# Kernel tuning notes

Hardware: AMD Instinct MI355X
Metric: run time of the kernel (lower is better)

Reference implementation:

```python
import jax, jax.numpy as jnp
import numpy as np

B, N, K, F, S = 128, 116, 4, 72, 8
TOPK = 10
INTRA_T, INTER_T = 0.1, 0.2


def _safe_corr(f):
    # f: [batch, d, m] -> corr [batch, d, d], matching torch _safe_compute_correlation
    c = f - f.mean(axis=2, keepdims=True)
    cov = jnp.einsum('bim,bjm->bij', c, c)
    var = jnp.diagonal(cov, axis1=1, axis2=2)
    std = jnp.sqrt(jnp.clip(var, 1e-8, None))[:, :, None]
    corr = cov / (std * std.transpose(0, 2, 1) + 1e-8)
    return jnp.clip(corr, -1.0, 1.0)


def _sym(m):
    return (m + m.swapaxes(-1, -2)) * 0.5


def setup_inputs():
    key = jax.random.key(0)
    ks = jax.random.split(key, 8)
    def lin(k, out_d, in_d):
        return jax.random.normal(k, (out_d, in_d), jnp.float32) * (1.0 / np.sqrt(in_d))
    return {
        'band_features': jax.random.normal(ks[0], (B, N, K, F), jnp.float32),
        'attn_weights': jax.random.uniform(ks[1], (B, N, S, K), jnp.float32),
        'intra_thresh_adj': jnp.zeros((), jnp.float32),
        'inter_thresh_adj': jnp.zeros((), jnp.float32),
        'attn_fuse_weight': jnp.asarray(0.5, jnp.float32),
        'intra_W1': lin(ks[2], 64, N), 'intra_b1': jnp.zeros((64,), jnp.float32),
        'intra_W2': lin(ks[3], N, 64), 'intra_b2': jnp.zeros((N,), jnp.float32),
        'inter_W1': lin(ks[4], 32, K), 'inter_b1': jnp.zeros((32,), jnp.float32),
        'inter_W2': lin(ks[5], K, 32), 'inter_b2': jnp.zeros((K,), jnp.float32),
        'comp_W': lin(ks[6], 128, 2 * F + 6), 'comp_b': jnp.zeros((128,), jnp.float32),
    }


def reference(band_features, attn_weights, intra_thresh_adj, inter_thresh_adj,
              attn_fuse_weight, intra_W1, intra_b1, intra_W2, intra_b2,
              inter_W1, inter_b1, inter_W2, inter_b2, comp_W, comp_b):
    dt = band_features.dtype
    # ---- intra-band graph: [B*K, N, N] correlations ----
    x = band_features.transpose(0, 2, 1, 3).reshape(B * K, N, F)
    corr = _safe_corr(x)
    th = INTRA_T + jax.nn.sigmoid(intra_thresh_adj) * 0.2
    tmask = (jnp.abs(corr) > th).astype(dt)
    _, idx = jax.lax.top_k(jnp.abs(corr), min(TOPK, N))  # [B*K, N, k]
    bix = jnp.arange(B * K)[:, None, None]
    rix = jnp.arange(N)[None, :, None]
    kmask = jnp.zeros_like(corr).at[bix, rix, idx].set(1.0)
    sc = jax.nn.relu(_sym(corr * tmask * kmask))
    h = jax.nn.relu(sc.reshape(-1, N) @ intra_W1.T + intra_b1)  # dropout = eval identity
    intra = jax.nn.sigmoid(h @ intra_W2.T + intra_b2).reshape(B * K, N, N)
    intra_adj = _sym(intra).reshape(B, K, N, N)
    # ---- inter-band graph: [B*N, K, K] correlations ----
    y = band_features.reshape(B * N, K, F)
    base = _safe_corr(y)
    a = attn_weights.reshape(B * N, S, K).transpose(0, 2, 1)  # [B*N, K, S]
    acorr = _safe_corr(a)
    fw = jax.nn.sigmoid(attn_fuse_weight)
    base = fw * base + (1.0 - fw) * acorr
    th2 = INTER_T + jax.nn.sigmoid(inter_thresh_adj) * 0.2
    sc2 = jax.nn.relu(_sym(base * (jnp.abs(base) > th2).astype(dt)))
    h2 = jax.nn.relu(sc2.reshape(-1, K) @ inter_W1.T + inter_b1)
    inter = jax.nn.sigmoid(h2 @ inter_W2.T + inter_b2).reshape(B * N, K, K)
    inter_adj = _sym(inter).reshape(B, N, K, K)
    # ---- unified graph assembly (vectorized replacement of nested loops) ----
    kk = jnp.arange(K)
    bd = jnp.zeros((B, K, N, K, N), dt).at[:, kk, :, kk, :].set(
        intra_adj.transpose(1, 0, 2, 3))  # block-diagonal intra blocks
    unified = bd.reshape(B, K * N, K * N)
    kk1, kk2, nn = np.meshgrid(np.arange(K), np.arange(K), np.arange(N), indexing='ij')
    sel = (kk1 != kk2).ravel()
    k1f, k2f, nf = kk1.ravel()[sel], kk2.ravel()[sel], nn.ravel()[sel]
    vals = inter_adj[:, nf, k1f, k2f]  # [B, M]
    unified_adj = unified.at[:, k1f * N + nf, k2f * N + nf].set(vals)
    # ---- node features ----
    node_features = band_features.transpose(0, 2, 1, 3).reshape(B, K * N, F)
    # ---- graph-level features ----
    node_mean = band_features.mean(axis=(1, 2))
    node_std = jnp.std(band_features, axis=(1, 2), ddof=1)  # torch unbiased std
    deg = (intra_adj > 0).astype(dt).sum(axis=3)  # [B, K, N]
    tri = jnp.einsum('bkij,bkji->bki', intra_adj, intra_adj)  # diag of A@A
    clus = tri / (deg ** 2 + 1e-8)
    dens = (inter_adj > 0).astype(dt).mean(axis=(2, 3))  # [B, N]
    stren = inter_adj.mean(axis=(2, 3))
    gf = jnp.concatenate([
        node_mean, node_std,
        deg.mean(axis=(1, 2))[:, None], jnp.std(deg, axis=(1, 2), ddof=1)[:, None],
        clus.mean(axis=(1, 2))[:, None], jnp.std(clus, axis=(1, 2), ddof=1)[:, None],
        dens.mean(axis=1)[:, None], stren.mean(axis=1)[:, None]], axis=1)
    graph_features = jax.nn.relu(gf @ comp_W.T + comp_b)
    # ---- sparsity scalars ----
    intra_sp = 1.0 - (intra_adj > 0).astype(dt).mean()
    inter_sp = 1.0 - (inter_adj > 0).astype(dt).mean()
    it, jt = float(B * K * N * N), float(B * N * K * K)
    total_sp = (intra_sp * it + inter_sp * jt) / (it + jt)
    return (unified_adj, node_features, graph_features, intra_adj, inter_adj,
            intra_sp, inter_sp, total_sp)
```

## Files before the change

kernel.cpp:

```cpp
#include <hip/hip_runtime.h>
#include <math.h>

#define NB 128
#define NN_ 116
#define NK 4
#define NF 72
#define NS 8
#define TOPK 10

#define BK (NB*NK)
#define BN (NB*NN_)
#define NN2 (NN_*NN_)
#define KN (NK*NN_)
#define ROWS (BK*NN_)

#define OFF_UNI 0
#define SZ_UNI (NB*KN*KN)
#define OFF_NF (OFF_UNI + SZ_UNI)
#define SZ_NF (NB*KN*NF)
#define OFF_GF (OFF_NF + SZ_NF)
#define SZ_GF (NB*128)
#define OFF_IA (OFF_GF + SZ_GF)
#define SZ_IA (NB*NK*NN_*NN_)
#define OFF_IE (OFF_IA + SZ_IA)
#define SZ_IE (NB*NN_*NK*NK)
#define OFF_SP (OFF_IE + SZ_IE)

#define SCR_CORR 0
#define SCR_DEG (SCR_CORR + SZ_IA)
#define SCR_CLUS (SCR_DEG + ROWS)
#define SCR_DENS (SCR_CLUS + ROWS)
#define SCR_STREN (SCR_DENS + BN)
#define SCR_AUX (SCR_STREN + BN)

#define NFQ (SZ_NF/4)
#define UNQ (SZ_UNI/4)
#define NB_CORR 512
#define NB_INTER (BN/64)
#define NB_COPY 1044

__device__ __forceinline__ float sigmoidf_(float x){ return 1.0f/(1.0f+expf(-x)); }
__device__ __forceinline__ float dot4_(float4 a, float4 b){
    return fmaf(a.x,b.x, fmaf(a.y,b.y, fmaf(a.z,b.z, a.w*b.w)));
}
#define CLIP1(x) fminf(1.0f, fmaxf(-1.0f, (x)))

__global__ __launch_bounds__(256, 1) void k_corr_inter(const float* __restrict__ band,
    const float* __restrict__ attn, const float* __restrict__ thadj2,
    const float* __restrict__ fwp,
    const float* __restrict__ eW1, const float* __restrict__ eb1,
    const float* __restrict__ eW2, const float* __restrict__ eb2,
    float* __restrict__ corr_out, float* __restrict__ inter_out,
    float* __restrict__ dens_out, float* __restrict__ stren_out,
    float* __restrict__ nf)
{
    __shared__ float sx[NF*120];
    __shared__ float smu[120], srs[120];
    __shared__ float sW1[128], sb1[32], sW2[128], sb2[4];
    __shared__ float sMat[256*4];
    int t = threadIdx.x;
    if (blockIdx.x < NB_CORR){
        int bk = blockIdx.x;
        int b = bk >> 2, k = bk & 3;
        const float* xin = band + ((size_t)b*NN_*NK + k)*NF;
        for (int e = t; e < NN_*NF; e += 256){
            int n = e / NF, f = e - n*NF;
            sx[f*120 + n] = xin[(size_t)n*NK*NF + f];
        }
        for (int e = t; e < NF*4; e += 256)
            sx[(e>>2)*120 + NN_ + (e&3)] = 0.0f;
        __syncthreads();
        if (t < NN_){
            float s = 0.f, ss = 0.f;
            for (int f = 0; f < NF; ++f){ float v = sx[f*120+t]; s += v; ss += v*v; }
            float mu = s * (1.0f/NF);
            float sd = sqrtf(fmaxf(ss - s*mu, 1e-8f));
            smu[t] = mu; srs[t] = 1.0f/sd;
        }
        __syncthreads();
        for (int e = t; e < NF*NN_; e += 256){
            int f = e / NN_, n = e - f*NN_;
            sx[f*120+n] = (sx[f*120+n] - smu[n]) * srs[n];
        }
        __syncthreads();
        float* dst = corr_out + (size_t)bk * NN2;
        if (t < 225){
            int ti = t / 15, tj = t - ti*15;
            int i0 = ti*8, j0 = tj*8;
            float acc[8][8] = {};
            for (int f = 0; f < NF; ++f){
                const float4 a0 = *(const float4*)&sx[f*120 + i0];
                const float4 a1 = *(const float4*)&sx[f*120 + i0 + 4];
                const float4 c0 = *(const float4*)&sx[f*120 + j0];
                const float4 c1 = *(const float4*)&sx[f*120 + j0 + 4];
                float av[8] = {a0.x,a0.y,a0.z,a0.w,a1.x,a1.y,a1.z,a1.w};
                float cv[8] = {c0.x,c0.y,c0.z,c0.w,c1.x,c1.y,c1.z,c1.w};
                #pragma unroll
                for (int r = 0; r < 8; ++r)
                    #pragma unroll
                    for (int c = 0; c < 8; ++c)
                        acc[r][c] = fmaf(av[r], cv[c], acc[r][c]);
            }
            #pragma unroll
            for (int r = 0; r < 8; ++r){
                int i = i0 + r;
                if (i < NN_){
                    float4 v0;
                    v0.x = CLIP1(acc[r][0]); v0.y = CLIP1(acc[r][1]);
                    v0.z = CLIP1(acc[r][2]); v0.w = CLIP1(acc[r][3]);
                    *(float4*)&dst[i*NN_ + j0] = v0;
                    if (j0 + 4 <= 112){
                        float4 v1;
                        v1.x = CLIP1(acc[r][4]); v1.y = CLIP1(acc[r][5]);
                        v1.z = CLIP1(acc[r][6]); v1.w = CLIP1(acc[r][7]);
                        *(float4*)&dst[i*NN_ + j0 + 4] = v1;
                    }
                }
            }
        }
    } else if (blockIdx.x < NB_CORR + NB_INTER){
        if (t < 128) sW1[t] = eW1[t];
        if (t < 32) sb1[t] = eb1[t];
        if (t >= 128 && t < 256) sW2[t-128] = eW2[t-128];
        if (t < 4) sb2[t] = eb2[t];
        __syncthreads();
        int l = t & 3;
        int il = t >> 2;
        size_t item = (size_t)(blockIdx.x - NB_CORR)*64 + il;

        const float* xr = band + item*(NK*NF) + l*NF;
        float s=0,p0=0,p1=0,p2=0,p3=0;
        for (int f = 0; f < NF; ++f){
            float v = xr[f];
            float v1=__shfl_xor(v,1), v2=__shfl_xor(v,2), v3=__shfl_xor(v,3);
            s += v; p0=fmaf(v,v,p0); p1=fmaf(v,v1,p1); p2=fmaf(v,v2,p2); p3=fmaf(v,v3,p3);
        }
        float mu = s*(1.0f/NF);
        float mu1=__shfl_xor(mu,1), mu2=__shfl_xor(mu,2), mu3=__shfl_xor(mu,3);
        float sd = sqrtf(fmaxf(p0 - s*mu, 1e-8f));
        float sd1=__shfl_xor(sd,1), sd2=__shfl_xor(sd,2), sd3=__shfl_xor(sd,3);
        float c0 = CLIP1((p0 - (float)NF*mu*mu )/(sd*sd +1e-8f));
        float c1 = CLIP1((p1 - (float)NF*mu*mu1)/(sd*sd1+1e-8f));
        float c2 = CLIP1((p2 - (float)NF*mu*mu2)/(sd*sd2+1e-8f));
        float c3 = CLIP1((p3 - (float)NF*mu*mu3)/(sd*sd3+1e-8f));

        const float* ar = attn + item*(NS*NK) + l;
        float as=0,q0=0,q1=0,q2=0,q3=0;
        #pragma unroll
        for (int s8 = 0; s8 < NS; ++s8){
            float v = ar[s8*NK];
            float v1=__shfl_xor(v,1), v2=__shfl_xor(v,2), v3=__shfl_xor(v,3);
            as += v; q0=fmaf(v,v,q0); q1=fmaf(v,v1,q1); q2=fmaf(v,v2,q2); q3=fmaf(v,v3,q3);
        }
        float am = as*(1.0f/NS);
        float am1=__shfl_xor(am,1), am2=__shfl_xor(am,2), am3=__shfl_xor(am,3);
        float ad = sqrtf(fmaxf(q0 - as*am, 1e-8f));
        float ad1=__shfl_xor(ad,1), ad2=__shfl_xor(ad,2), ad3=__shfl_xor(ad,3);
        float a0 = CLIP1((q0 - (float)NS*am*am )/(ad*ad +1e-8f));
        float a1 = CLIP1((q1 - (float)NS*am*am1)/(ad*ad1+1e-8f));
        float a2 = CLIP1((q2 - (float)NS*am*am2)/(ad*ad2+1e-8f));
        float a3 = CLIP1((q3 - (float)NS*am*am3)/(ad*ad3+1e-8f));

        float fwv = sigmoidf_(fwp[0]);
        float g0 = fwv*c0 + (1.0f-fwv)*a0;
        float g1 = fwv*c1 + (1.0f-fwv)*a1;
        float g2 = fwv*c2 + (1.0f-fwv)*a2;
        float g3 = fwv*c3 + (1.0f-fwv)*a3;
        float th2 = 0.2f + sigmoidf_(thadj2[0])*0.2f;
        float m0 = (fabsf(g0)>th2)?g0:0.f;
        float m1 = (fabsf(g1)>th2)?g1:0.f;
        float m2 = (fabsf(g2)>th2)?g2:0.f;
        float m3 = (fabsf(g3)>th2)?g3:0.f;

        sMat[il*16 + l*4 + (l^0)] = m0;
        sMat[il*16 + l*4 + (l^1)] = m1;
        sMat[il*16 + l*4 + (l^2)] = m2;
        sMat[il*16 + l*4 + (l^3)] = m3;
        __syncthreads();
        float x0 = fmaxf(0.5f*(sMat[il*16 + l*4 + 0] + sMat[il*16 + 0*4 + l]), 0.f);
        float x1 = fmaxf(0.5f*(sMat[il*16 + l*4 + 1] + sMat[il*16 + 1*4 + l]), 0.f);
        float x2 = fmaxf(0.5f*(sMat[il*16 + l*4 + 2] + sMat[il*16 + 2*4 + l]), 0.f);
        float x3 = fmaxf(0.5f*(sMat[il*16 + l*4 + 3] + sMat[il*16 + 3*4 + l]), 0.f);

        float h[32];
        #pragma unroll
        for (int o = 0; o < 32; ++o){
            float acc = sb1[o];
            acc = fmaf(sW1[o*4+0], x0, acc);
            acc = fmaf(sW1[o*4+1], x1, acc);
            acc = fmaf(sW1[o*4+2], x2, acc);
            acc = fmaf(sW1[o*4+3], x3, acc);
            h[o] = fmaxf(acc, 0.f);
        }
        float o0=sb2[0], o1=sb2[1], o2=sb2[2], o3=sb2[3];
        #pragma unroll
        for (int o = 0; o < 32; ++o){
            float hv = h[o];
            o0 = fmaf(sW2[0*32+o], hv, o0);
            o1 = fmaf(sW2[1*32+o], hv, o1);
            o2 = fmaf(sW2[2*32+o], hv, o2);
            o3 = fmaf(sW2[3*32+o], hv, o3);
        }
        o0 = sigmoidf_(o0); o1 = sigmoidf_(o1); o2 = sigmoidf_(o2); o3 = sigmoidf_(o3);
        __syncthreads();
        sMat[il*16 + l*4 + 0] = o0;
        sMat[il*16 + l*4 + 1] = o1;
        sMat[il*16 + l*4 + 2] = o2;
        sMat[il*16 + l*4 + 3] = o3;
        __syncthreads();
        float y0 = 0.5f*(o0 + sMat[il*16 + 0*4 + l]);
        float y1 = 0.5f*(o1 + sMat[il*16 + 1*4 + l]);
        float y2 = 0.5f*(o2 + sMat[il*16 + 2*4 + l]);
        float y3 = 0.5f*(o3 + sMat[il*16 + 3*4 + l]);
        *(float4*)&inter_out[item*16 + l*4] = make_float4(y0,y1,y2,y3);

        float cnt = ((y0>0.f)?1.f:0.f) + ((y1>0.f)?1.f:0.f) + ((y2>0.f)?1.f:0.f) + ((y3>0.f)?1.f:0.f);
        float sum = y0+y1+y2+y3;
        cnt += __shfl_xor(cnt,1); cnt += __shfl_xor(cnt,2);
        sum += __shfl_xor(sum,1); sum += __shfl_xor(sum,2);
        if (l == 0){
            dens_out[item]  = cnt * (1.0f/16.0f);
            stren_out[item] = sum * (1.0f/16.0f);
        }
    } else {
        int gid = (blockIdx.x - NB_CORR - NB_INTER)*256 + t;
        int gsz = NB_COPY*256;
        for (int q = gid; q < NFQ; q += gsz){
            int fq = q % 18;
            int rest = q / 18;
            int b = rest / KN;
            int p = rest - b*KN;
            int k = p / NN_;
            int n = p - k*NN_;
            float4 v = *(const float4*)&band[(((size_t)b*NN_ + n)*NK + k)*NF + fq*4];
            *(float4*)&nf[(size_t)q*4] = v;
        }
    }
}

__global__ __launch_bounds__(1024, 1) void k_topk_mlpsym(const float* __restrict__ corr,
    const float* __restrict__ thadj,
    const float* __restrict__ W1, const float* __restrict__ b1,
    const float* __restrict__ W2, const float* __restrict__ b2,
    float* __restrict__ ia, float* __restrict__ deg_out, float* __restrict__ clus_out)
{
    __shared__ float smem[38708];
    float* sA  = smem;
    float* sB  = smem + 14036;
    float* sW2 = smem + 21460;
    float* sH  = smem + 30164;
    float* sb1 = smem + 38052;
    float* sb2 = smem + 38116;
    unsigned* sKm  = (unsigned*)(smem + 38244);
    unsigned* sTop = (unsigned*)sH;
    int bk = blockIdx.x, t = threadIdx.x;

    const float* src = corr + (size_t)bk*NN2;
    for (int e4 = t; e4 < NN2/4; e4 += 1024){
        int e = e4*4;
        int i = e / 116, j = e - i*116;
        float4 v = *(const float4*)&src[e];
        sA[i*121 + j + 0] = v.x;
        sA[i*121 + j + 1] = v.y;
        sA[i*121 + j + 2] = v.z;
        sA[i*121 + j + 3] = v.w;
    }
    for (int e4 = t; e4 < 1856; e4 += 1024)
        *(float4*)&sB[e4*4] = *(const float4*)&W1[e4*4];
    for (int e = t; e < 128*64; e += 1024){
        int j = e >> 6, o = e & 63;
        sW2[j*68 + o] = (j < NN_) ? W2[e] : 0.0f;
    }
    if (t < 64) sb1[t] = b1[t];
    if (t >= 64 && t < 192) sb2[t-64] = (t-64 < NN_) ? b2[t-64] : 0.0f;
    __syncthreads();

    if (t < 464){
        int r = t >> 2, q = t & 3;
        const float* row = &sA[r*121 + q*29];
        int jbase = q*29;
        unsigned tv[TOPK];
        #pragma unroll
        for (int p = 0; p < TOPK; ++p) tv[p] = 0u;
        for (int jj = 0; jj < 29; ++jj){
            float c = fabsf(row[jj]);
            unsigned u = (__float_as_uint(c) & 0xFFFFFF80u) | (unsigned)(127 - (jbase + jj));
            #pragma unroll
            for (int p = 0; p < TOPK; ++p){
                unsigned old = tv[p];
                bool gt = u > old;
                tv[p] = gt ? u : old;
                u = gt ? old : u;
            }
        }
        #pragma unroll
        for (int p = 0; p < TOPK; ++p) sTop[t*10 + p] = tv[p];
    }
    __syncthreads();

    if (t < NN_){
        const unsigned* L0 = &sTop[(4*t+0)*10];
        const unsigned* L1 = &sTop[(4*t+1)*10];
        const unsigned* L2 = &sTop[(4*t+2)*10];
        const unsigned* L3 = &sTop[(4*t+3)*10];
        int i0=0, i1=0, i2=0, i3=0;
        unsigned m0=0,m1=0,m2=0,m3=0;
        #pragma unroll
        for (int p = 0; p < TOPK; ++p){
            unsigned u0 = L0[i0], u1 = L1[i1], u2 = L2[i2], u3 = L3[i3];
            unsigned ua = u0 > u1 ? u0 : u1;
            unsigned ub = u2 > u3 ? u2 : u3;
            unsigned u  = ua > ub ? ua : ub;
            if (u == u0) ++i0; else if (u == u1) ++i1; else if (u == u2) ++i2; else ++i3;
            int j = 127 - (int)(u & 127u);
            unsigned bit = 1u << (j & 31);
            int w = j >> 5;
            if (w == 0) m0 |= bit; else if (w == 1) m1 |= bit; else if (w == 2) m2 |= bit; else m3 |= bit;
        }
        sKm[t*4+0]=m0; sKm[t*4+1]=m1; sKm[t*4+2]=m2; sKm[t*4+3]=m3;
    }
    __syncthreads();

    {
        float th = 0.1f + sigmoidf_(thadj[0]) * 0.2f;
        float vb[14];
        #pragma unroll
        for (int it = 0; it < 14; ++it){
            int e = t + it*1024;
            float v = 0.0f;
            if (e < NN2){
                int i = e / 116, j = e - i*116;
                float cij = sA[i*121 + j];
                float cji = sA[j*121 + i];
                bool kij = (sKm[i*4 + (j>>5)] >> (j&31)) & 1u;
                bool kji = (sKm[j*4 + (i>>5)] >> (i&31)) & 1u;
                float mij = (fabsf(cij) > th && kij) ? cij : 0.0f;
                float mji = (fabsf(cji) > th && kji) ? cji : 0.0f;
                v = fmaxf(0.5f*(mij+mji), 0.0f);
            }
            vb[it] = v;
        }
        __syncthreads();
        #pragma unroll
        for (int it = 0; it < 14; ++it){
            int e = t + it*1024;
            if (e < NN2) sA[e] = vb[it];
        }
    }
    __syncthreads();

    if (t < 928){
        int rg = t >> 4, og = t & 15;
        float acc[2][4] = {};
        for (int j4 = 0; j4 < 29; ++j4){
            float4 s[2], w[4];
            #pragma unroll
            for (int m = 0; m < 2; ++m) s[m] = *(const float4*)&sA[(rg+58*m)*116 + j4*4];
            #pragma unroll
            for (int n = 0; n < 4; ++n) w[n] = *(const float4*)&sB[(og+16*n)*116 + j4*4];
            #pragma unroll
            for (int m = 0; m < 2; ++m)
                #pragma unroll
                for (int n = 0; n < 4; ++n)
                    acc[m][n] += dot4_(s[m], w[n]);
        }
        #pragma unroll
        for (int m = 0; m < 2; ++m)
            #pragma unroll
            for (int n = 0; n < 4; ++n)
                sH[(rg+58*m)*68 + og+16*n] = fmaxf(acc[m][n] + sb1[og+16*n], 0.0f);
    }
    __syncthreads();

    if (t < 928){
        int rg = t >> 4, jg = t & 15;
        float acc[2][8] = {};
        for (int o4 = 0; o4 < 16; ++o4){
            float4 h[2], w[8];
            #pragma unroll
            for (int m = 0; m < 2; ++m) h[m] = *(const float4*)&sH[(rg+58*m)*68 + o4*4];
            #pragma unroll
            for (int q = 0; q < 8; ++q) w[q] = *(const float4*)&sW2[(jg+16*q)*68 + o4*4];
            #pragma unroll
            for (int m = 0; m < 2; ++m)
                #pragma unroll
                for (int q = 0; q < 8; ++q)
                    acc[m][q] += dot4_(h[m], w[q]);
        }
        #pragma unroll
        for (int m = 0; m < 2; ++m){
            int row = rg + 58*m;
            #pragma unroll
            for (int q = 0; q < 8; ++q){
                int j = jg + 16*q;
                if (j < NN_)
                    sA[row*121 + j] = sigmoidf_(acc[m][q] + sb2[j]);
            }
        }
    }
    __syncthreads();

    float* dia = ia + (size_t)bk*NN2;
    for (int e4 = t; e4 < NN2/4; e4 += 1024){
        int e = e4*4;
        int i = e / 116, j0 = e - i*116;
        float4 v;
        v.x = 0.5f*(sA[i*121+j0+0] + sA[(j0+0)*121+i]);
        v.y = 0.5f*(sA[i*121+j0+1] + sA[(j0+1)*121+i]);
        v.z = 0.5f*(sA[i*121+j0+2] + sA[(j0+2)*121+i]);
        v.w = 0.5f*(sA[i*121+j0+3] + sA[(j0+3)*121+i]);
        *(float4*)&dia[e] = v;
    }
    if (t < 464){
        int r = t >> 2, q = t & 3;
        float tri = 0.f, dg = 0.f;
        for (int jj = 0; jj < 29; ++jj){
            int j = q*29 + jj;
            float v = 0.5f*(sA[r*121+j] + sA[j*121+r]);
            tri = fmaf(v, v, tri);
            dg += (v > 0.f) ? 1.f : 0.f;
        }
        tri += __shfl_xor(tri,1); tri += __shfl_xor(tri,2);
        dg  += __shfl_xor(dg,1);  dg  += __shfl_xor(dg,2);
        if (q == 0){
            deg_out[(size_t)bk*NN_ + r]  = dg;
            clus_out[(size_t)bk*NN_ + r] = tri / (dg*dg + 1e-8f);
        }
    }
}

__global__ __launch_bounds__(256) void k_gstats_lin(const float* __restrict__ band,
    const float* __restrict__ deg, const float* __restrict__ clus,
    const float* __restrict__ dens, const float* __restrict__ stren,
    const float* __restrict__ Wc, const float* __restrict__ bc,
    float* __restrict__ gfo, float* __restrict__ aux)
{
    int b = blockIdx.x, t = threadIdx.x;
    __shared__ float sGf[152];
    __shared__ float sPs[18*14*4];
    __shared__ float sPq[18*14*4];
    __shared__ float sA[4], sB[4];

    if (t < 252){
        int fq = t % 18, g = t / 18;
        float4 s = make_float4(0,0,0,0), q = make_float4(0,0,0,0);
        const float* base = band + (size_t)b*(KN*NF);
        for (int nk = g; nk < KN; nk += 14){
            float4 v = *(const float4*)&base[nk*NF + fq*4];
            s.x += v.x; s.y += v.y; s.z += v.z; s.w += v.w;
            q.x = fmaf(v.x,v.x,q.x); q.y = fmaf(v.y,v.y,q.y);
            q.z = fmaf(v.z,v.z,q.z); q.w = fmaf(v.w,v.w,q.w);
        }
        int idx = (fq*14 + g)*4;
        *(float4*)&sPs[idx] = s;
        *(float4*)&sPq[idx] = q;
    }
    __syncthreads();
    if (t < NF){
        int fq = t >> 2, e = t & 3;
        float S = 0.f, Q = 0.f;
        for (int g = 0; g < 14; ++g){ S += sPs[(fq*14+g)*4+e]; Q += sPq[(fq*14+g)*4+e]; }
        float mean = S * (1.0f/(float)KN);
        float var = fmaxf((Q - S*mean)/((float)KN - 1.0f), 0.0f);
        sGf[t] = mean;
        sGf[NF + t] = sqrtf(var);
    }
    __syncthreads();

    float s = 0.f, ss = 0.f;
    for (int e = t; e < KN; e += 256){ float v = deg[(size_t)b*KN + e]; s += v; ss += v*v; }
    #pragma unroll
    for (int d = 1; d < 64; d <<= 1){ s += __shfl_xor(s,d); ss += __shfl_xor(ss,d); }
    if ((t & 63) == 0){ sA[t>>6] = s; sB[t>>6] = ss; }
    __syncthreads();
    if (t == 0){
        float S0 = sA[0]+sA[1]+sA[2]+sA[3], S1 = sB[0]+sB[1]+sB[2]+sB[3];
        float Mv = (float)KN, mean = S0/Mv;
        float var = fmaxf((S1 - S0*mean)/(Mv - 1.0f), 0.0f);
        sGf[144] = mean; sGf[145] = sqrtf(var);
        aux[b] = S0;
    }
    __syncthreads();

    s = 0.f; ss = 0.f;
    for (int e = t; e < KN; e += 256){ float v = clus[(size_t)b*KN + e]; s += v; ss += v*v; }
    #pragma unroll
    for (int d = 1; d < 64; d <<= 1){ s += __shfl_xor(s,d); ss += __shfl_xor(ss,d); }
    if ((t & 63) == 0){ sA[t>>6] = s; sB[t>>6] = ss; }
    __syncthreads();
    if (t == 0){
        float S0 = sA[0]+sA[1]+sA[2]+sA[3], S1 = sB[0]+sB[1]+sB[2]+sB[3];
        float Mv = (float)KN, mean = S0/Mv;
        float var = fmaxf((S1 - S0*mean)/(Mv - 1.0f), 0.0f);
        sGf[146] = mean; sGf[147] = sqrtf(var);
    }
    __syncthreads();

    s = 0.f; ss = 0.f;
    for (int e = t; e < NN_; e += 256){ s += dens[(size_t)b*NN_ + e]; ss += stren[(size_t)b*NN_ + e]; }
    #pragma unroll
    for (int d = 1; d < 64; d <<= 1){ s += __shfl_xor(s,d); ss += __shfl_xor(ss,d); }
    if ((t & 63) == 0){ sA[t>>6] = s; sB[t>>6] = ss; }
    __syncthreads();
    if (t == 0){
        float S0 = sA[0]+sA[1]+sA[2]+sA[3], S1 = sB[0]+sB[1]+sB[2]+sB[3];
        sGf[148] = S0 / (float)NN_;
        sGf[149] = S1 / (float)NN_;
        aux[128 + b] = S0 * 16.0f;
    }
    __syncthreads();

    if (t < 128){
        float acc = bc[t];
        const float* w = Wc + (size_t)t*150;
        for (int c = 0; c < 150; ++c) acc = fmaf(sGf[c], w[c], acc);
        gfo[(size_t)b*128 + t] = fmaxf(acc, 0.f);
    }
}

__global__ __launch_bounds__(64) void k_sparsity(const float* __restrict__ aux, float* __restrict__ out3)
{
    int t = threadIdx.x;
    float a = aux[t] + aux[64 + t];
    float c = aux[128 + t] + aux[192 + t];
    #pragma unroll
    for (int d = 1; d < 64; d <<= 1){ a += __shfl_xor(a,d); c += __shfl_xor(c,d); }
    if (t == 0){
        const float it = 6889472.0f, jt = 237568.0f;
        float isp = 1.0f - a/it;
        float jsp = 1.0f - c/jt;
        out3[0] = isp; out3[1] = jsp;
        out3[2] = (isp*it + jsp*jt)/(it + jt);
    }
}

__global__ __launch_bounds__(256) void k_uninf(const float* __restrict__ intra_adj,
    const float* __restrict__ inter_adj, const float* __restrict__ aux,
    float* __restrict__ uni, float* __restrict__ sp, int do_sp)
{
    if (do_sp && blockIdx.x == 0 && threadIdx.x < 64){
        int t = threadIdx.x;
        float a = aux[t] + aux[64 + t];
        float c = aux[128 + t] + aux[192 + t];
        #pragma unroll
        for (int d = 1; d < 64; d <<= 1){ a += __shfl_xor(a,d); c += __shfl_xor(c,d); }
        if (t == 0){
            const float it = 6889472.0f, jt = 237568.0f;
            float isp = 1.0f - a/it;
            float jsp = 1.0f - c/jt;
            sp[0] = isp; sp[1] = jsp;
            sp[2] = (isp*it + jsp*jt)/(it + jt);
        }
    }
    int gid = blockIdx.x*256 + threadIdx.x;
    int gsz = gridDim.x*256;
    for (int q = gid; q < UNQ; q += gsz){
        int row = q / 116;
        int cq  = q - row*116;
        int b = row / KN;
        int p = row - b*KN;
        int k1 = p / NN_;
        int i  = p - k1*NN_;
        int k2 = cq / 29;
        int j0 = cq*4 - k2*NN_;
        float4 v;
        if (k2 == k1){
            v = *(const float4*)&intra_adj[(((size_t)b*NK + k1)*NN_ + i)*NN_ + j0];
        } else {
            int d = i - j0;
            float val = 0.f;
            if (d >= 0 && d < 4)
                val = inter_adj[(((size_t)b*NN_ + i)*NK + k1)*NK + k2];
            v.x = (d==0)?val:0.f;
            v.y = (d==1)?val:0.f;
            v.z = (d==2)?val:0.f;
            v.w = (d==3)?val:0.f;
        }
        *(float4*)&uni[(size_t)q*4] = v;
    }
}

extern "C" void kernel_launch(void* const* d_in, const int* in_sizes, int n_in,
                              void* d_out, int out_size, void* d_ws, size_t ws_size,
                              hipStream_t stream)
{
    const float* band = (const float*)d_in[0];
    const float* attn = (const float*)d_in[1];
    const float* thA  = (const float*)d_in[2];
    const float* thE  = (const float*)d_in[3];
    const float* fw   = (const float*)d_in[4];
    const float* iW1  = (const float*)d_in[5];
    const float* ib1  = (const float*)d_in[6];
    const float* iW2  = (const float*)d_in[7];
    const float* ib2  = (const float*)d_in[8];
    const float* eW1  = (const float*)d_in[9];
    const float* eb1  = (const float*)d_in[10];
    const float* eW2  = (const float*)d_in[11];
    const float* eb2  = (const float*)d_in[12];
    const float* cW   = (const float*)d_in[13];
    const float* cb   = (const float*)d_in[14];

    float* out = (float*)d_out;
    float* uni = out + OFF_UNI;
    float* nf  = out + OFF_NF;
    float* gfo = out + OFF_GF;
    float* ia  = out + OFF_IA;
    float* ie  = out + OFF_IE;
    float* sp  = out + OFF_SP;

    float* scr_corr  = uni + SCR_CORR;
    float* scr_deg   = uni + SCR_DEG;
    float* scr_clus  = uni + SCR_CLUS;
    float* scr_dens  = uni + SCR_DENS;
    float* scr_stren = uni + SCR_STREN;

    int ws_ok = (ws_size >= 256*sizeof(float));
    float* aux = ws_ok ? (float*)d_ws : (uni + SCR_AUX);

    k_corr_inter<<<NB_CORR + NB_INTER + NB_COPY, 256, 0, stream>>>(
        band, attn, thE, fw, eW1, eb1, eW2, eb2,
        scr_corr, ie, scr_dens, scr_stren, nf);
    k_topk_mlpsym<<<BK, 1024, 0, stream>>>(scr_corr, thA, iW1, ib1, iW2, ib2,
                                           ia, scr_deg, scr_clus);
    k_gstats_lin<<<NB, 256, 0, stream>>>(band, scr_deg, scr_clus, scr_dens, scr_stren,
                                         cW, cb, gfo, aux);
    if (!ws_ok)
        k_sparsity<<<1, 64, 0, stream>>>(aux, sp);
    k_uninf<<<2048, 256, 0, stream>>>(ia, ie, aux, uni, sp, ws_ok ? 1 : 0);
}
```

Baseline: 140.0 us.

## Split-K the intra MLP matmuls across thread pairs with padded LDS strides

The two small per-graph MLP matmuls in the top-k/MLP kernel now give each thread a 4-row register tile (instead of 2) and split the reduction dimension between adjacent lanes, combined with a shuffle-xor. W1 and W2 shared-memory rows are padded (120 and 76 floats) to change bank mapping. This is meant to increase register-level reuse of weight loads and reduce LDS traffic and bank conflicts. In exchange it needs more registers per thread in a 1024-thread block and adds shuffle reductions.

Measured after the change: 144.6 us. 3.3% more time.

```diff
diff --git a/kernel.cpp b/kernel.cpp
--- a/kernel.cpp
+++ b/kernel.cpp
@@ -244,14 +244,14 @@
     const float* __restrict__ W2, const float* __restrict__ b2,
     float* __restrict__ ia, float* __restrict__ deg_out, float* __restrict__ clus_out)
 {
-    __shared__ float smem[38708];
+    __shared__ float smem[39988];
     float* sA  = smem;
-    float* sB  = smem + 14036;
-    float* sW2 = smem + 21460;
-    float* sH  = smem + 30164;
-    float* sb1 = smem + 38052;
-    float* sb2 = smem + 38116;
-    unsigned* sKm  = (unsigned*)(smem + 38244);
+    float* sW1 = smem + 14036;
+    float* sW2 = smem + 21716;
+    float* sH  = smem + 31444;
+    float* sb1 = smem + 39332;
+    float* sb2 = smem + 39396;
+    unsigned* sKm  = (unsigned*)(smem + 39524);
     unsigned* sTop = (unsigned*)sH;
     int bk = blockIdx.x, t = threadIdx.x;
 
@@ -265,11 +265,14 @@
         sA[i*121 + j + 2] = v.z;
         sA[i*121 + j + 3] = v.w;
     }
-    for (int e4 = t; e4 < 1856; e4 += 1024)
-        *(float4*)&sB[e4*4] = *(const float4*)&W1[e4*4];
+    for (int e4 = t; e4 < 1856; e4 += 1024){
+        int e = e4*4;
+        int o = e / 116, j = e - o*116;
+        *(float4*)&sW1[o*120 + j] = *(const float4*)&W1[e];
+    }
     for (int e = t; e < 128*64; e += 1024){
         int j = e >> 6, o = e & 63;
-        sW2[j*68 + o] = (j < NN_) ? W2[e] : 0.0f;
+        sW2[j*76 + o] = (j < NN_) ? W2[e] : 0.0f;
     }
     if (t < 64) sb1[t] = b1[t];
     if (t >= 64 && t < 192) sb2[t-64] = (t-64 < NN_) ? b2[t-64] : 0.0f;
@@ -350,51 +353,69 @@
     __syncthreads();
 
     if (t < 928){
-        int rg = t >> 4, og = t & 15;
-        float acc[2][4] = {};
-        for (int j4 = 0; j4 < 29; ++j4){
-            float4 s[2], w[4];
-            #pragma unroll
-            for (int m = 0; m < 2; ++m) s[m] = *(const float4*)&sA[(rg+58*m)*116 + j4*4];
-            #pragma unroll
-            for (int n = 0; n < 4; ++n) w[n] = *(const float4*)&sB[(og+16*n)*116 + j4*4];
-            #pragma unroll
-            for (int m = 0; m < 2; ++m)
+        int base = t >> 1, kh = t & 1;
+        int rg = base >> 4, og = base & 15;
+        int j4b = kh ? 15 : 0, j4e = kh ? 29 : 15;
+        float acc[4][4] = {};
+        for (int j4 = j4b; j4 < j4e; ++j4){
+            float4 s[4], w[4];
+            #pragma unroll
+            for (int m = 0; m < 4; ++m) s[m] = *(const float4*)&sA[(rg+29*m)*116 + j4*4];
+            #pragma unroll
+            for (int n = 0; n < 4; ++n) w[n] = *(const float4*)&sW1[(og+16*n)*120 + j4*4];
+            #pragma unroll
+            for (int m = 0; m < 4; ++m)
                 #pragma unroll
                 for (int n = 0; n < 4; ++n)
                     acc[m][n] += dot4_(s[m], w[n]);
         }
         #pragma unroll
-        for (int m = 0; m < 2; ++m)
+        for (int m = 0; m < 4; ++m)
             #pragma unroll
             for (int n = 0; n < 4; ++n)
-                sH[(rg+58*m)*68 + og+16*n] = fmaxf(acc[m][n] + sb1[og+16*n], 0.0f);
+                acc[m][n] += __shfl_xor(acc[m][n], 1);
+        if (kh == 0){
+            #pragma unroll
+            for (int m = 0; m < 4; ++m)
+                #pragma unroll
+                for (int n = 0; n < 4; ++n)
+                    sH[(rg+29*m)*68 + og+16*n] = fmaxf(acc[m][n] + sb1[og+16*n], 0.0f);
+        }
     }
     __syncthreads();
 
     if (t < 928){
-        int rg = t >> 4, jg = t & 15;
-        float acc[2][8] = {};
-        for (int o4 = 0; o4 < 16; ++o4){
-            float4 h[2], w[8];
-            #pragma unroll
-            for (int m = 0; m < 2; ++m) h[m] = *(const float4*)&sH[(rg+58*m)*68 + o4*4];
-            #pragma unroll
-            for (int q = 0; q < 8; ++q) w[q] = *(const float4*)&sW2[(jg+16*q)*68 + o4*4];
-            #pragma unroll
-            for (int m = 0; m < 2; ++m)
+        int base = t >> 1, kh = t & 1;
+        int rg = base >> 4, jg = base & 15;
+        int o4b = kh * 8;
+        float acc[4][8] = {};
+        for (int o4 = o4b; o4 < o4b + 8; ++o4){
+            float4 h[4], w[8];
+            #pragma unroll
+            for (int m = 0; m < 4; ++m) h[m] = *(const float4*)&sH[(rg+29*m)*68 + o4*4];
+            #pragma unroll
+            for (int q = 0; q < 8; ++q) w[q] = *(const float4*)&sW2[(jg+16*q)*76 + o4*4];
+            #pragma unroll
+            for (int m = 0; m < 4; ++m)
                 #pragma unroll
                 for (int q = 0; q < 8; ++q)
                     acc[m][q] += dot4_(h[m], w[q]);
         }
         #pragma unroll
-        for (int m = 0; m < 2; ++m){
-            int row = rg + 58*m;
-            #pragma unroll
-            for (int q = 0; q < 8; ++q){
-                int j = jg + 16*q;
-                if (j < NN_)
-                    sA[row*121 + j] = sigmoidf_(acc[m][q] + sb2[j]);
+        for (int m = 0; m < 4; ++m)
+            #pragma unroll
+            for (int q = 0; q < 8; ++q)
+                acc[m][q] += __shfl_xor(acc[m][q], 1);
+        if (kh == 0){
+            #pragma unroll
+            for (int m = 0; m < 4; ++m){
+                int row = rg + 29*m;
+                #pragma unroll
+                for (int q = 0; q < 8; ++q){
+                    int j = jg + 16*q;
+                    if (j < NN_)
+                        sA[row*121 + j] = sigmoidf_(acc[m][q] + sb2[j]);
+                }
             }
         }
     }
```
